# Performance work log

Measured on AMD Instinct MI355X. Metric: run time of the kernel, lower is better.

## Reference

```python
import jax, jax.numpy as jnp
import numpy as np

B, T, C = 2, 1024, 1024
I = 4096          # intermediate_size
E = 8             # num_experts
TOP_K = 2


def setup_inputs() -> dict:
    key = jax.random.key(0)
    ks = jax.random.split(key, 14)
    s = lambda fan_in: 1.0 / np.sqrt(fan_in)
    inp = {
        "x": jax.random.normal(ks[0], (B, T, C), jnp.float32),
        # router: Linear(C, C//4) -> ReLU -> Linear(C//4, E)
        "rw1": jax.random.normal(ks[1], (C, C // 4), jnp.float32) * s(C),
        "rb1": jnp.zeros((C // 4,), jnp.float32),
        "rw2": jax.random.normal(ks[2], (C // 4, E), jnp.float32) * s(C // 4),
        "rb2": jnp.zeros((E,), jnp.float32),
        # experts: E x (Linear(C, I) -> SiLU -> Linear(I, C))
        "ew1": jax.random.normal(ks[3], (E, C, I), jnp.float32) * s(C),
        "eb1": jnp.zeros((E, I), jnp.float32),
        "ew2": jax.random.normal(ks[4], (E, I, C), jnp.float32) * s(I),
        "eb2": jnp.zeros((E, C), jnp.float32),
        # shared expert
        "sw1": jax.random.normal(ks[5], (C, I), jnp.float32) * s(C),
        "sb1": jnp.zeros((I,), jnp.float32),
        "sw2": jax.random.normal(ks[6], (I, C), jnp.float32) * s(I),
        "sb2": jnp.zeros((C,), jnp.float32),
    }
    return inp


def reference(x, rw1, rb1, rw2, rb2, ew1, eb1, ew2, eb2, sw1, sb1, sw2, sb2):
    N = B * T
    xf = x.reshape(N, C)

    # router -> softmax gates over experts
    logits = jax.nn.relu(xf @ rw1 + rb1) @ rw2 + rb2          # [N, E]
    gates = jax.nn.softmax(logits, axis=-1)

    # top-k selection, then re-softmax of (gate / top_k)
    topk_gates, topk_idx = jax.lax.top_k(gates, TOP_K)        # [N, K]
    topk_gates = jax.nn.softmax(topk_gates / TOP_K, axis=-1)

    # combine weights per (token, expert); top-k indices are distinct per token
    comb = jnp.zeros((N, E), xf.dtype).at[
        jnp.arange(N)[:, None], topk_idx].add(topk_gates)     # [N, E]

    # dense expert compute (all experts for all tokens), masked combine
    h = jax.nn.silu(jnp.einsum('nc,eci->nei', xf, ew1) + eb1)  # [N, E, I]
    eout = jnp.einsum('nei,eic->nec', h, ew2) + eb2            # [N, E, C]
    expert_mix = jnp.einsum('nec,ne->nc', eout, comb)          # [N, C]

    shared = jax.nn.silu(xf @ sw1 + sb1) @ sw2 + sb2           # [N, C]

    return (shared + expert_mix).reshape(B, T, C)
```

## Files before the change

kernel.cpp:

```cpp
#include <hip/hip_runtime.h>
#include <cstdint>
#include <cstddef>
#include <cstdio>

#define DI __device__ __forceinline__

typedef __attribute__((ext_vector_type(4))) float f32x4;
typedef __attribute__((ext_vector_type(8))) short bf16x8;

static constexpr int TOK  = 2048;
static constexpr int CDIM = 1024;
static constexpr int IDIM = 4096;
static constexpr int RHID = 256;
static constexpr int RK   = 4096;
static constexpr int PAIR_CAP = 2048 + 4096 + 8 * 128;

DI float bf2f(unsigned short u) {
  unsigned int v = ((unsigned int)u) << 16;
  float f; __builtin_memcpy(&f, &v, sizeof(f));
  return f;
}
DI unsigned short f2bf(float f) {
  unsigned int u; __builtin_memcpy(&u, &f, sizeof(u));
  u += 0x7fffu + ((u >> 16) & 1u);
  return (unsigned short)(u >> 16);
}

DI void gload16(const unsigned short* g, unsigned short* l) {
  unsigned short* gm = const_cast<unsigned short*>(g);
  __builtin_amdgcn_global_load_lds(
      (__attribute__((address_space(1))) void*)gm,
      (__attribute__((address_space(3))) void*)l, 16, 0, 0);
}

__global__ void cvt_x_k(const float* __restrict__ x, unsigned short* __restrict__ xb,
                        unsigned short* __restrict__ xcat) {
  const int i = (blockIdx.x * 256 + threadIdx.x) * 4;
  const float4 v = *(const float4*)(x + i);
  unsigned short hi[4], lo[4];
  const float vf[4] = {v.x, v.y, v.z, v.w};
#pragma unroll
  for (int j = 0; j < 4; ++j) {
    hi[j] = f2bf(vf[j]);
    lo[j] = f2bf(vf[j] - bf2f(hi[j]));
  }
  const int row = i >> 10, col = i & 1023;
  *(uint2*)(xb + (size_t)row * CDIM + col) = *(const uint2*)hi;
  unsigned short* xr = xcat + (size_t)row * RK;
  *(uint2*)(xr + col)        = *(const uint2*)hi;
  *(uint2*)(xr + col + 1024) = *(const uint2*)hi;
  *(uint2*)(xr + col + 2048) = *(const uint2*)lo;
  *(uint2*)(xr + col + 3072) = *(const uint2*)lo;
}

__global__ void transpose_f2b_k(const float* __restrict__ src, unsigned short* __restrict__ dst,
                                int R, int Cc) {
  __shared__ float tile[64][65];
  src += (size_t)blockIdx.z * R * Cc;
  dst += (size_t)blockIdx.z * R * Cc;
  const int c0 = blockIdx.x * 64, r0 = blockIdx.y * 64;
  const int t = threadIdx.x;
  const int tr = t >> 4, tc = (t & 15) * 4;
#pragma unroll
  for (int it = 0; it < 4; ++it) {
    const int r = tr + it * 16;
    const float4 v = *(const float4*)(src + (size_t)(r0 + r) * Cc + c0 + tc);
    tile[r][tc] = v.x; tile[r][tc + 1] = v.y; tile[r][tc + 2] = v.z; tile[r][tc + 3] = v.w;
  }
  __syncthreads();
  const int j0 = (t & 7) * 8;
#pragma unroll
  for (int it = 0; it < 2; ++it) {
    const int cl = (t >> 3) + it * 32;
    unsigned short tmp[8];
#pragma unroll
    for (int j = 0; j < 8; ++j) tmp[j] = f2bf(tile[j0 + j][cl]);
    *(uint4*)(dst + (size_t)(c0 + cl) * R + r0 + j0) = *(const uint4*)tmp;
  }
}

__global__ void router_w_prep(const float* __restrict__ src, unsigned short* __restrict__ dst) {
  __shared__ float tile[64][65];
  const int Cc = RHID;
  const int c0 = blockIdx.x * 64, r0 = blockIdx.y * 64;
  const int t = threadIdx.x;
  const int tr = t >> 4, tc = (t & 15) * 4;
#pragma unroll
  for (int it = 0; it < 4; ++it) {
    const int r = tr + it * 16;
    const float4 v = *(const float4*)(src + (size_t)(r0 + r) * Cc + c0 + tc);
    tile[r][tc] = v.x; tile[r][tc + 1] = v.y; tile[r][tc + 2] = v.z; tile[r][tc + 3] = v.w;
  }
  __syncthreads();
  const int j0 = (t & 7) * 8;
#pragma unroll
  for (int it = 0; it < 2; ++it) {
    const int cl = (t >> 3) + it * 32;
    unsigned short hi[8], lo[8];
#pragma unroll
    for (int j = 0; j < 8; ++j) {
      const float v = tile[j0 + j][cl];
      hi[j] = f2bf(v);
      lo[j] = f2bf(v - bf2f(hi[j]));
    }
    unsigned short* dr = dst + (size_t)(c0 + cl) * RK + r0 + j0;
    *(uint4*)(dr)        = *(const uint4*)hi;
    *(uint4*)(dr + 1024) = *(const uint4*)lo;
    *(uint4*)(dr + 2048) = *(const uint4*)hi;
    *(uint4*)(dr + 3072) = *(const uint4*)lo;
  }
}

__global__ void zero_f32(float4* __restrict__ p) {
  p[(size_t)blockIdx.x * 256 + threadIdx.x] = make_float4(0.f, 0.f, 0.f, 0.f);
}

__global__ void init_meta(int* __restrict__ meta, int* __restrict__ pair_token) {
  const int i = blockIdx.x * 256 + threadIdx.x;
  if (i < 64) meta[i] = 0;
  if (i < PAIR_CAP) pair_token[i] = (i < TOK) ? i : 0;
}

__global__ void router_finish(const float* __restrict__ rh,
                              const float* __restrict__ rw2,
                              const float* __restrict__ rb2,
                              int* __restrict__ tok_e, float* __restrict__ tok_w,
                              int* __restrict__ meta) {
  const int wave = threadIdx.x >> 6, lane = threadIdx.x & 63;
  const int t = blockIdx.x * 4 + wave;
  float a[8] = {0, 0, 0, 0, 0, 0, 0, 0};
  const float* hp = rh + (size_t)t * RHID;
#pragma unroll
  for (int it = 0; it < 4; ++it) {
    const int j = it * 64 + lane;
    const float hv = fmaxf(hp[j], 0.0f);
    const float4 wa = *(const float4*)(rw2 + (size_t)j * 8);
    const float4 wb = *(const float4*)(rw2 + (size_t)j * 8 + 4);
    a[0] += hv * wa.x; a[1] += hv * wa.y; a[2] += hv * wa.z; a[3] += hv * wa.w;
    a[4] += hv * wb.x; a[5] += hv * wb.y; a[6] += hv * wb.z; a[7] += hv * wb.w;
  }
#pragma unroll
  for (int off = 32; off > 0; off >>= 1)
#pragma unroll
    for (int e = 0; e < 8; ++e) a[e] += __shfl_down(a[e], off);
  if (lane == 0) {
    float lg[8], mx = -1e30f;
#pragma unroll
    for (int e = 0; e < 8; ++e) { lg[e] = a[e] + rb2[e]; mx = fmaxf(mx, lg[e]); }
    float s = 0.f;
#pragma unroll
    for (int e = 0; e < 8; ++e) { lg[e] = __expf(lg[e] - mx); s += lg[e]; }
    const float inv = 1.f / s;
#pragma unroll
    for (int e = 0; e < 8; ++e) lg[e] *= inv;
    int e1 = 0; float g1 = lg[0];
#pragma unroll
    for (int e = 1; e < 8; ++e) if (lg[e] > g1) { g1 = lg[e]; e1 = e; }
    int e2 = -1; float g2 = -1e30f;
#pragma unroll
    for (int e = 0; e < 8; ++e) if (e != e1 && lg[e] > g2) { g2 = lg[e]; e2 = e; }
    const float eb = __expf((g2 - g1) * 0.5f);
    const float w1 = 1.f / (1.f + eb), w2 = eb / (1.f + eb);
    tok_e[2 * t] = e1; tok_e[2 * t + 1] = e2;
    tok_w[2 * t] = w1; tok_w[2 * t + 1] = w2;
    atomicAdd(&meta[e1], 1); atomicAdd(&meta[e2], 1);
  }
}

__global__ void compute_offsets(int* __restrict__ meta) {
  if (threadIdx.x == 0) {
    int o = TOK;
    for (int e = 0; e < 8; ++e) {
      meta[16 + e] = o;
      const int tl = (meta[e] + 127) >> 7;
      meta[32 + e] = tl;
      o += tl << 7;
    }
  }
}

__global__ void scatter_pairs(const int* __restrict__ tok_e, int* __restrict__ meta,
                              int* __restrict__ pair_token, int* __restrict__ pair_pos) {
  const int t = blockIdx.x * 256 + threadIdx.x;
#pragma unroll
  for (int k = 0; k < 2; ++k) {
    const int e = tok_e[2 * t + k];
    const int pos = meta[16 + e] + atomicAdd(&meta[8 + e], 1);
    pair_token[pos] = t;
    pair_pos[2 * t + k] = pos;
  }
}

template <int MODE, int ACT, bool OUTF32, int SPLIT>
__global__ __launch_bounds__(256) void gemm128(
    const unsigned short* __restrict__ A,
    const unsigned short* __restrict__ BtE, const unsigned short* __restrict__ BtS,
    const float* __restrict__ biasE, const float* __restrict__ biasS,
    void* __restrict__ Cout,
    const int* __restrict__ meta, const int* __restrict__ pair_token,
    int N, int K) {
  __shared__ unsigned short Alds[3][128 * 32];
  __shared__ unsigned short Blds[3][128 * 32];

  const int tid = threadIdx.x, wave = tid >> 6, lane = tid & 63;

  int ks = 0, zz = blockIdx.z;
  if (MODE == 0) {
    ks = zz;
  } else if (SPLIT > 1) {
    ks = zz / 9; zz -= ks * 9;
  }

  const unsigned short* Bt;
  const float* bias;
  int row0;
  if (MODE == 0) {
    row0 = blockIdx.y * 128; Bt = BtE; bias = biasE;
  } else {
    if (zz < 8) {
      if ((int)blockIdx.y >= meta[32 + zz]) return;
      row0 = meta[16 + zz] + blockIdx.y * 128;
      Bt = BtE + (size_t)zz * N * K;
      bias = biasE + zz * N;
    } else {
      row0 = blockIdx.y * 128;
      Bt = BtS; bias = biasS;
    }
  }
  const int n0 = blockIdx.x * 128;
  const int Kc = K / SPLIT;
  const size_t kbase = (size_t)ks * Kc;

  const unsigned short* aSrc[2];
  const unsigned short* bSrc[2];
  int ldsOff[2];
#pragma unroll
  for (int i = 0; i < 2; ++i) {
    const int q = i * 256 + tid;
    const int m = q >> 2;
    const int c = (q & 3) ^ ((m >> 1) & 3);
    const size_t arow = (MODE == 1) ? (size_t)pair_token[row0 + m] : (size_t)(row0 + m);
    aSrc[i] = A + arow * K + kbase + c * 8;
    bSrc[i] = Bt + (size_t)(n0 + m) * K + kbase + c * 8;
    ldsOff[i] = q * 8;
  }

  const int wr = wave >> 1, wc = wave & 1;
  int aOff[4], bOff[4];
#pragma unroll
  for (int t = 0; t < 4; ++t) {
    const int ar = wr * 64 + t * 16 + (lane & 15);
    aOff[t] = (ar * 4 + ((lane >> 4) ^ ((ar >> 1) & 3))) * 8;
    const int br = wc * 64 + t * 16 + (lane & 15);
    bOff[t] = (br * 4 + ((lane >> 4) ^ ((br >> 1) & 3))) * 8;
  }

  f32x4 acc[4][4] = {};
  const int kIters = Kc >> 5;

#pragma unroll
  for (int i = 0; i < 2; ++i) {
    gload16(aSrc[i], &Alds[0][ldsOff[i]]);
    gload16(bSrc[i], &Blds[0][ldsOff[i]]);
  }
  if (kIters > 1) {
#pragma unroll
    for (int i = 0; i < 2; ++i) {
      gload16(aSrc[i] + 32, &Alds[1][ldsOff[i]]);
      gload16(bSrc[i] + 32, &Blds[1][ldsOff[i]]);
    }
  }

  int cur = 0;
  for (int kk = 0; kk < kIters; ++kk) {
    if (kk + 1 < kIters) asm volatile("s_waitcnt vmcnt(4)" ::: "memory");
    else                 asm volatile("s_waitcnt vmcnt(0)" ::: "memory");
    __builtin_amdgcn_s_barrier();
    asm volatile("" ::: "memory");
    if (kk + 2 < kIters) {
      int ib = cur + 2; if (ib >= 3) ib -= 3;
      const int ko = (kk + 2) * 32;
#pragma unroll
      for (int i = 0; i < 2; ++i) {
        gload16(aSrc[i] + ko, &Alds[ib][ldsOff[i]]);
        gload16(bSrc[i] + ko, &Blds[ib][ldsOff[i]]);
      }
    }
    bf16x8 af[4], bfr[4];
#pragma unroll
    for (int t = 0; t < 4; ++t) {
      af[t]  = *(const bf16x8*)(&Alds[cur][aOff[t]]);
      bfr[t] = *(const bf16x8*)(&Blds[cur][bOff[t]]);
    }
    __builtin_amdgcn_s_setprio(1);
#pragma unroll
    for (int mt = 0; mt < 4; ++mt)
#pragma unroll
      for (int nt = 0; nt < 4; ++nt)
        acc[mt][nt] = __builtin_amdgcn_mfma_f32_16x16x32_bf16(af[mt], bfr[nt], acc[mt][nt], 0, 0, 0);
    __builtin_amdgcn_s_setprio(0);
    ++cur; if (cur >= 3) cur = 0;
  }

  float bv[4];
  const bool addb = (SPLIT == 1) || (ks == 0);
#pragma unroll
  for (int nt = 0; nt < 4; ++nt)
    bv[nt] = addb ? bias[n0 + wc * 64 + nt * 16 + (lane & 15)] : 0.0f;

  const int rb = row0 + wr * 64 + ((lane >> 4) * 4);
  const int cb = n0 + wc * 64 + (lane & 15);
#pragma unroll
  for (int mt = 0; mt < 4; ++mt)
#pragma unroll
    for (int nt = 0; nt < 4; ++nt)
#pragma unroll
      for (int r = 0; r < 4; ++r) {
        float v = acc[mt][nt][r] + bv[nt];
        if (ACT == 1) v = fmaxf(v, 0.0f);
        if (ACT == 2) v = v / (1.0f + __expf(-v));
        const size_t idx = (size_t)(rb + mt * 16 + r) * (size_t)N + (size_t)(cb + nt * 16);
        if (SPLIT > 1)   atomicAdd((float*)Cout + idx, v);
        else if (OUTF32) ((float*)Cout)[idx] = v;
        else             ((unsigned short*)Cout)[idx] = f2bf(v);
      }
}

__global__ void combine_out(const float* __restrict__ op, const int* __restrict__ pair_pos,
                            const float* __restrict__ tok_w, float* __restrict__ y) {
  const int t = blockIdx.x;
  const int c = threadIdx.x * 4;
  const int p0 = pair_pos[2 * t], p1 = pair_pos[2 * t + 1];
  const float w0 = tok_w[2 * t], w1 = tok_w[2 * t + 1];
  const float4 vs = *(const float4*)(op + (size_t)t  * CDIM + c);
  const float4 va = *(const float4*)(op + (size_t)p0 * CDIM + c);
  const float4 vb = *(const float4*)(op + (size_t)p1 * CDIM + c);
  float4 o;
  o.x = vs.x + w0 * va.x + w1 * vb.x;
  o.y = vs.y + w0 * va.y + w1 * vb.y;
  o.z = vs.z + w0 * va.z + w1 * vb.z;
  o.w = vs.w + w0 * va.w + w1 * vb.w;
  *(float4*)(y + (size_t)t * CDIM + c) = o;
}

extern "C" void kernel_launch(void* const* d_in, const int* in_sizes, int n_in,
                              void* d_out, int out_size, void* d_ws, size_t ws_size,
                              hipStream_t stream) {
  const float* x   = (const float*)d_in[0];
  const float* rw1 = (const float*)d_in[1];
  const float* rb1 = (const float*)d_in[2];
  const float* rw2 = (const float*)d_in[3];
  const float* rb2 = (const float*)d_in[4];
  const float* ew1 = (const float*)d_in[5];
  const float* eb1 = (const float*)d_in[6];
  const float* ew2 = (const float*)d_in[7];
  const float* eb2 = (const float*)d_in[8];
  const float* sw1 = (const float*)d_in[9];
  const float* sb1 = (const float*)d_in[10];
  const float* sw2 = (const float*)d_in[11];
  const float* sb2 = (const float*)d_in[12];

  char* w = (char*)d_ws;
  auto alloc = [&](size_t bytes) {
    char* p = w; w += (bytes + 255) & ~(size_t)255; return p;
  };
  unsigned short* ew1T = (unsigned short*)alloc(8ull * IDIM * CDIM * 2);
  unsigned short* ew2T = (unsigned short*)alloc(8ull * CDIM * IDIM * 2);
  unsigned short* sw1T = (unsigned short*)alloc((size_t)IDIM * CDIM * 2);
  unsigned short* sw2T = (unsigned short*)alloc((size_t)CDIM * IDIM * 2);
  unsigned short* h    = (unsigned short*)alloc((size_t)PAIR_CAP * IDIM * 2);
  float* op            = (float*)alloc((size_t)PAIR_CAP * CDIM * 4);
  float* tok_w         = (float*)alloc(2 * TOK * 4);
  int*   tok_e         = (int*)alloc(2 * TOK * 4);
  int*   meta          = (int*)alloc(64 * 4);
  int*   pair_token    = (int*)alloc(PAIR_CAP * 4);
  int*   pair_pos      = (int*)alloc(2 * TOK * 4);
  const size_t need = (size_t)(w - (char*)d_ws);
  if (need > ws_size) {
    fprintf(stderr, "kernel_launch: ws too small: need %zu have %zu\n", need, ws_size);
    return;
  }
  unsigned short* xcat = (unsigned short*)h;
  unsigned short* wcat = (unsigned short*)((char*)op);
  float*          rh   = (float*)((char*)op + (4ull << 20));
  unsigned short* xb   = (unsigned short*)((char*)op + (8ull << 20));

  cvt_x_k<<<TOK * CDIM / 1024, 256, 0, stream>>>(x, xb, xcat);
  router_w_prep<<<dim3(RHID / 64, CDIM / 64, 1), 256, 0, stream>>>(rw1, wcat);
  transpose_f2b_k<<<dim3(IDIM / 64, CDIM / 64, 8), 256, 0, stream>>>(ew1, ew1T, CDIM, IDIM);
  transpose_f2b_k<<<dim3(CDIM / 64, IDIM / 64, 8), 256, 0, stream>>>(ew2, ew2T, IDIM, CDIM);
  transpose_f2b_k<<<dim3(IDIM / 64, CDIM / 64, 1), 256, 0, stream>>>(sw1, sw1T, CDIM, IDIM);
  transpose_f2b_k<<<dim3(CDIM / 64, IDIM / 64, 1), 256, 0, stream>>>(sw2, sw2T, IDIM, CDIM);

  init_meta<<<PAIR_CAP / 256, 256, 0, stream>>>(meta, pair_token);

  zero_f32<<<TOK * RHID / 1024, 256, 0, stream>>>((float4*)rh);
  gemm128<0, 0, true, 8><<<dim3(RHID / 128, TOK / 128, 8), 256, 0, stream>>>(
      xcat, wcat, nullptr, rb1, nullptr, rh, nullptr, nullptr, RHID, RK);
  router_finish<<<TOK / 4, 256, 0, stream>>>(rh, rw2, rb2, tok_e, tok_w, meta);
  compute_offsets<<<1, 64, 0, stream>>>(meta);
  scatter_pairs<<<TOK / 256, 256, 0, stream>>>(tok_e, meta, pair_token, pair_pos);

  gemm128<1, 2, false, 1><<<dim3(IDIM / 128, 16, 9), 256, 0, stream>>>(
      xb, ew1T, sw1T, eb1, sb1, h, meta, pair_token, IDIM, CDIM);
  zero_f32<<<PAIR_CAP * CDIM / 1024, 256, 0, stream>>>((float4*)op);
  gemm128<2, 0, true, 2><<<dim3(CDIM / 128, 16, 18), 256, 0, stream>>>(
      h, ew2T, sw2T, eb2, sb2, op, meta, nullptr, CDIM, IDIM);

  combine_out<<<TOK, 256, 0, stream>>>(op, pair_pos, tok_w, (float*)d_out);
}
```

Before: 698.4 us.

## Replace split-K atomics with per-slab stores and reduce slabs in consumers

Split-K GEMMs now write each K-slice into its own fp32 slab with plain stores instead of atomicAdd into a zeroed buffer. Router_finish sums the eight router slabs and combine_out sums the two expert-output slabs. This removes the zero-fill kernels and atomic traffic, at the cost of doubling the op workspace and extra reads in the consumers. It also swaps the LDS fragment loads to inline ds_read_b128 with explicit waitcnt and sched barriers.

```diff
diff --git a/kernel.cpp b/kernel.cpp
--- a/kernel.cpp
+++ b/kernel.cpp
@@ -7,6 +7,7 @@
 
 typedef __attribute__((ext_vector_type(4))) float f32x4;
 typedef __attribute__((ext_vector_type(8))) short bf16x8;
+typedef __attribute__((address_space(3))) const unsigned short* lds_cp;
 
 static constexpr int TOK  = 2048;
 static constexpr int CDIM = 1024;
@@ -109,10 +110,6 @@
     *(uint4*)(dr + 2048) = *(const uint4*)hi;
     *(uint4*)(dr + 3072) = *(const uint4*)lo;
   }
-}
-
-__global__ void zero_f32(float4* __restrict__ p) {
-  p[(size_t)blockIdx.x * 256 + threadIdx.x] = make_float4(0.f, 0.f, 0.f, 0.f);
 }
 
 __global__ void init_meta(int* __restrict__ meta, int* __restrict__ pair_token) {
@@ -133,7 +130,10 @@
 #pragma unroll
   for (int it = 0; it < 4; ++it) {
     const int j = it * 64 + lane;
-    const float hv = fmaxf(hp[j], 0.0f);
+    float hv = hp[j];
+#pragma unroll
+    for (int s = 1; s < 8; ++s) hv += hp[j + (size_t)s * TOK * RHID];
+    hv = fmaxf(hv, 0.0f);
     const float4 wa = *(const float4*)(rw2 + (size_t)j * 8);
     const float4 wb = *(const float4*)(rw2 + (size_t)j * 8 + 4);
     a[0] += hv * wa.x; a[1] += hv * wa.y; a[2] += hv * wa.z; a[3] += hv * wa.w;
@@ -198,7 +198,7 @@
     const float* __restrict__ biasE, const float* __restrict__ biasS,
     void* __restrict__ Cout,
     const int* __restrict__ meta, const int* __restrict__ pair_token,
-    int N, int K) {
+    int N, int K, int slabStride) {
   __shared__ unsigned short Alds[3][128 * 32];
   __shared__ unsigned short Blds[3][128 * 32];
 
@@ -276,7 +276,6 @@
     if (kk + 1 < kIters) asm volatile("s_waitcnt vmcnt(4)" ::: "memory");
     else                 asm volatile("s_waitcnt vmcnt(0)" ::: "memory");
     __builtin_amdgcn_s_barrier();
-    asm volatile("" ::: "memory");
     if (kk + 2 < kIters) {
       int ib = cur + 2; if (ib >= 3) ib -= 3;
       const int ko = (kk + 2) * 32;
@@ -289,9 +288,11 @@
     bf16x8 af[4], bfr[4];
 #pragma unroll
     for (int t = 0; t < 4; ++t) {
-      af[t]  = *(const bf16x8*)(&Alds[cur][aOff[t]]);
-      bfr[t] = *(const bf16x8*)(&Blds[cur][bOff[t]]);
-    }
+      asm volatile("ds_read_b128 %0, %1" : "=v"(af[t])  : "v"((lds_cp)&Alds[cur][aOff[t]]));
+      asm volatile("ds_read_b128 %0, %1" : "=v"(bfr[t]) : "v"((lds_cp)&Blds[cur][bOff[t]]));
+    }
+    asm volatile("s_waitcnt lgkmcnt(0)" ::: "memory");
+    __builtin_amdgcn_sched_barrier(0);
     __builtin_amdgcn_s_setprio(1);
 #pragma unroll
     for (int mt = 0; mt < 4; ++mt)
@@ -299,6 +300,7 @@
       for (int nt = 0; nt < 4; ++nt)
         acc[mt][nt] = __builtin_amdgcn_mfma_f32_16x16x32_bf16(af[mt], bfr[nt], acc[mt][nt], 0, 0, 0);
     __builtin_amdgcn_s_setprio(0);
+    __builtin_amdgcn_sched_barrier(0);
     ++cur; if (cur >= 3) cur = 0;
   }
 
@@ -310,6 +312,7 @@
 
   const int rb = row0 + wr * 64 + ((lane >> 4) * 4);
   const int cb = n0 + wc * 64 + (lane & 15);
+  float* outp = (float*)Cout + (size_t)ks * (size_t)slabStride;
 #pragma unroll
   for (int mt = 0; mt < 4; ++mt)
 #pragma unroll
@@ -320,9 +323,8 @@
         if (ACT == 1) v = fmaxf(v, 0.0f);
         if (ACT == 2) v = v / (1.0f + __expf(-v));
         const size_t idx = (size_t)(rb + mt * 16 + r) * (size_t)N + (size_t)(cb + nt * 16);
-        if (SPLIT > 1)   atomicAdd((float*)Cout + idx, v);
-        else if (OUTF32) ((float*)Cout)[idx] = v;
-        else             ((unsigned short*)Cout)[idx] = f2bf(v);
+        if (OUTF32) outp[idx] = v;
+        else        ((unsigned short*)Cout)[idx] = f2bf(v);
       }
 }
 
@@ -332,14 +334,18 @@
   const int c = threadIdx.x * 4;
   const int p0 = pair_pos[2 * t], p1 = pair_pos[2 * t + 1];
   const float w0 = tok_w[2 * t], w1 = tok_w[2 * t + 1];
-  const float4 vs = *(const float4*)(op + (size_t)t  * CDIM + c);
-  const float4 va = *(const float4*)(op + (size_t)p0 * CDIM + c);
-  const float4 vb = *(const float4*)(op + (size_t)p1 * CDIM + c);
+  const float* op1 = op + (size_t)PAIR_CAP * CDIM;
+  const float4 vs0 = *(const float4*)(op  + (size_t)t  * CDIM + c);
+  const float4 vs1 = *(const float4*)(op1 + (size_t)t  * CDIM + c);
+  const float4 va0 = *(const float4*)(op  + (size_t)p0 * CDIM + c);
+  const float4 va1 = *(const float4*)(op1 + (size_t)p0 * CDIM + c);
+  const float4 vb0 = *(const float4*)(op  + (size_t)p1 * CDIM + c);
+  const float4 vb1 = *(const float4*)(op1 + (size_t)p1 * CDIM + c);
   float4 o;
-  o.x = vs.x + w0 * va.x + w1 * vb.x;
-  o.y = vs.y + w0 * va.y + w1 * vb.y;
-  o.z = vs.z + w0 * va.z + w1 * vb.z;
-  o.w = vs.w + w0 * va.w + w1 * vb.w;
+  o.x = (vs0.x + vs1.x) + w0 * (va0.x + va1.x) + w1 * (vb0.x + vb1.x);
+  o.y = (vs0.y + vs1.y) + w0 * (va0.y + va1.y) + w1 * (vb0.y + vb1.y);
+  o.z = (vs0.z + vs1.z) + w0 * (va0.z + va1.z) + w1 * (vb0.z + vb1.z);
+  o.w = (vs0.w + vs1.w) + w0 * (va0.w + va1.w) + w1 * (vb0.w + vb1.w);
   *(float4*)(y + (size_t)t * CDIM + c) = o;
 }
 
@@ -369,7 +375,7 @@
   unsigned short* sw1T = (unsigned short*)alloc((size_t)IDIM * CDIM * 2);
   unsigned short* sw2T = (unsigned short*)alloc((size_t)CDIM * IDIM * 2);
   unsigned short* h    = (unsigned short*)alloc((size_t)PAIR_CAP * IDIM * 2);
-  float* op            = (float*)alloc((size_t)PAIR_CAP * CDIM * 4);
+  float* op            = (float*)alloc(2ull * PAIR_CAP * CDIM * 4);
   float* tok_w         = (float*)alloc(2 * TOK * 4);
   int*   tok_e         = (int*)alloc(2 * TOK * 4);
   int*   meta          = (int*)alloc(64 * 4);
@@ -382,8 +388,8 @@
   }
   unsigned short* xcat = (unsigned short*)h;
   unsigned short* wcat = (unsigned short*)((char*)op);
-  float*          rh   = (float*)((char*)op + (4ull << 20));
   unsigned short* xb   = (unsigned short*)((char*)op + (8ull << 20));
+  float*          rh   = (float*)((char*)op + (24ull << 20));
 
   cvt_x_k<<<TOK * CDIM / 1024, 256, 0, stream>>>(x, xb, xcat);
   router_w_prep<<<dim3(RHID / 64, CDIM / 64, 1), 256, 0, stream>>>(rw1, wcat);
@@ -394,18 +400,16 @@
 
   init_meta<<<PAIR_CAP / 256, 256, 0, stream>>>(meta, pair_token);
 
-  zero_f32<<<TOK * RHID / 1024, 256, 0, stream>>>((float4*)rh);
   gemm128<0, 0, true, 8><<<dim3(RHID / 128, TOK / 128, 8), 256, 0, stream>>>(
-      xcat, wcat, nullptr, rb1, nullptr, rh, nullptr, nullptr, RHID, RK);
+      xcat, wcat, nullptr, rb1, nullptr, rh, nullptr, nullptr, RHID, RK, TOK * RHID);
   router_finish<<<TOK / 4, 256, 0, stream>>>(rh, rw2, rb2, tok_e, tok_w, meta);
   compute_offsets<<<1, 64, 0, stream>>>(meta);
   scatter_pairs<<<TOK / 256, 256, 0, stream>>>(tok_e, meta, pair_token, pair_pos);
 
   gemm128<1, 2, false, 1><<<dim3(IDIM / 128, 16, 9), 256, 0, stream>>>(
-      xb, ew1T, sw1T, eb1, sb1, h, meta, pair_token, IDIM, CDIM);
-  zero_f32<<<PAIR_CAP * CDIM / 1024, 256, 0, stream>>>((float4*)op);
+      xb, ew1T, sw1T, eb1, sb1, h, meta, pair_token, IDIM, CDIM, 0);
   gemm128<2, 0, true, 2><<<dim3(CDIM / 128, 16, 18), 256, 0, stream>>>(
-      h, ew2T, sw2T, eb2, sb2, op, meta, nullptr, CDIM, IDIM);
+      h, ew2T, sw2T, eb2, sb2, op, meta, nullptr, CDIM, IDIM, PAIR_CAP * CDIM);
 
   combine_out<<<TOK, 256, 0, stream>>>(op, pair_pos, tok_w, (float*)d_out);
 }
```

Measured after the change: 646.2 us. -7.5%, faster.
